# Kernel tuning notes

Measured on AMD Instinct MI355X. Metric: run time of the kernel, lower is better.

The kernel has to match this reference:

```python
import jax, jax.numpy as jnp
import numpy as np

M, N, H, K1, K2, C, B = 100000, 14000, 256, 16, 32, 7, 64
EPS = 1e-8


def setup_inputs() -> dict:
    key = jax.random.key(0)
    ks = jax.random.split(key, 8)
    embeds = jax.random.normal(ks[0], (M, H), dtype=jnp.float32)
    idx = jax.random.randint(ks[1], (N,), 0, M, dtype=jnp.int32)
    neighbors = jax.random.randint(ks[2], (N, K1), 0, M, dtype=jnp.int32)
    neighbors_2hop = jax.random.randint(ks[3], (N, K2), 0, M, dtype=jnp.int32)
    labels = (jnp.arange(N, dtype=jnp.int32) % C)  # perfectly balanced, as averageemb requires
    # prompt params (downstreamprompt weights, xavier-uniform [1,H])
    lim = float(np.sqrt(6.0 / (1 + H)))
    w_self = jax.random.uniform(ks[4], (1, H), jnp.float32, -lim, lim)
    w_n = jax.random.uniform(ks[5], (1, H), jnp.float32, -lim, lim)
    w_n2 = jax.random.uniform(ks[6], (1, H), jnp.float32, -lim, lim)
    # metanet (PromptVector): bottleneck adapter H -> B -> H
    k7, k8 = jax.random.split(ks[7])
    W1 = jax.random.normal(k7, (H, B), jnp.float32) * (1.0 / np.sqrt(H))
    b1 = jnp.zeros((B,), jnp.float32)
    W2 = jax.random.normal(k8, (B, H), jnp.float32) * (1.0 / np.sqrt(B))
    b2 = jnp.zeros((H,), jnp.float32)
    return {"embeds": embeds, "w_self": w_self, "w_n": w_n, "w_n2": w_n2,
            "W1": W1, "b1": b1, "W2": W2, "b2": b2,
            "idx": idx, "neighbors": neighbors, "neighbors_2hop": neighbors_2hop,
            "labels": labels}


def _cos(a, b):
    # torch.cosine_similarity with eps=1e-8 (clamped norms)
    num = jnp.sum(a * b, axis=-1)
    na = jnp.maximum(jnp.sqrt(jnp.sum(a * a, axis=-1)), EPS)
    nb = jnp.maximum(jnp.sqrt(jnp.sum(b * b, axis=-1)), EPS)
    return num / (na * nb)


def reference(embeds, w_self, w_n, w_n2, W1, b1, W2, b2,
              idx, neighbors, neighbors_2hop, labels):
    center = embeds[idx]                         # [N,H]
    ce = w_self * center                         # selfprompt: [N,H]
    nb = jnp.nan_to_num(w_n * embeds[neighbors])              # [N,K1,H]
    nb2 = jnp.nan_to_num(w_n2 * embeds[neighbors_2hop])       # [N,K2,H]
    nb_all = jnp.concatenate([nb, nb2], axis=1)  # [N,K1+K2,H]
    sim = _cos(ce[:, None, :], nb_all)           # [N,K]
    w = jax.nn.softmax(sim, axis=-1)
    weighted_neighbors = jnp.einsum('nk,nkh->nh', w, nb_all)
    inputs = weighted_neighbors + ce             # (dropout = identity at eval)
    prompts = jax.nn.elu(inputs @ W1 + b1) @ W2 + b2  # metanet adapter
    rawret = prompts + ce                        # [N,H]
    # averageemb: per-class mean (labels balanced, N/C per class)
    per_class = N // C
    ave = jax.ops.segment_sum(rawret, labels, num_segments=C) / per_class  # [C,H]
    ret = jax.nn.softmax(_cos(rawret[:, None, :], ave[None, :, :]), axis=1)  # [N,C]
    return ret
```

## Files before the change

### kernel.cpp

```cpp
#include <hip/hip_runtime.h>
#include <hip/hip_bf16.h>
#include <math.h>

#define H 256
#define NR 14000
#define MR 100000
#define K1C 16
#define K2C 32
#define KT 48
#define CC 7
#define EPSF 1e-8f
#define GC1 128
#define CHUNK ((NR + GC1 - 1) / GC1)

typedef __attribute__((ext_vector_type(8))) unsigned short ushort8_t;

__device__ __forceinline__ float rdlane(float v, int l) {
    return __int_as_float(__builtin_amdgcn_readlane(__float_as_int(v), l));
}

__device__ __forceinline__ float dot4(const float4 a, const float4 b) {
    return a.x * b.x + a.y * b.y + a.z * b.z + a.w * b.w;
}

__device__ __forceinline__ unsigned short f2bf(float x) {
    __hip_bfloat16 h = __float2bfloat16(x);
    return *(unsigned short*)&h;
}

__global__ __launch_bounds__(256) void kE(const float* __restrict__ src,
                                          unsigned short* __restrict__ dst) {
    const size_t base = ((size_t)blockIdx.x * 256 + threadIdx.x) * 8;
    const float4 a = *(const float4*)(src + base);
    const float4 b = *(const float4*)(src + base + 4);
    ushort8_t o;
    o[0] = f2bf(a.x); o[1] = f2bf(a.y); o[2] = f2bf(a.z); o[3] = f2bf(a.w);
    o[4] = f2bf(b.x); o[5] = f2bf(b.y); o[6] = f2bf(b.z); o[7] = f2bf(b.w);
    *(ushort8_t*)(dst + base) = o;
}

__global__ __launch_bounds__(256) void kA2(
    const float* __restrict__ embeds, const unsigned short* __restrict__ ebf,
    const float* __restrict__ w_self, const float* __restrict__ w_n,
    const float* __restrict__ w_n2, const int* __restrict__ idx,
    const int* __restrict__ nbr1, const int* __restrict__ nbr2,
    float* __restrict__ inbuf, float* __restrict__ cebuf)
{
    const int tid = threadIdx.x;
    const int wv = tid >> 6, lane = tid & 63;
    const int n = blockIdx.x * 4 + wv;
    const int g = lane >> 4, l = lane & 15;
    const int hb = l * 16;

    float ce[16], wn[16], wn2[16];
    float na2 = 0.f;
    const int cidx = idx[n];
    const float* crow = embeds + (size_t)cidx * H + hb;
#pragma unroll
    for (int j = 0; j < 4; ++j) {
        const float4 wsv  = *(const float4*)(w_self + hb + 4 * j);
        const float4 wnv  = *(const float4*)(w_n    + hb + 4 * j);
        const float4 wn2v = *(const float4*)(w_n2   + hb + 4 * j);
        const float4 cv   = *(const float4*)(crow + 4 * j);
        wn[4*j+0] = wnv.x;  wn[4*j+1] = wnv.y;  wn[4*j+2] = wnv.z;  wn[4*j+3] = wnv.w;
        wn2[4*j+0] = wn2v.x; wn2[4*j+1] = wn2v.y; wn2[4*j+2] = wn2v.z; wn2[4*j+3] = wn2v.w;
        ce[4*j+0] = wsv.x * cv.x; ce[4*j+1] = wsv.y * cv.y;
        ce[4*j+2] = wsv.z * cv.z; ce[4*j+3] = wsv.w * cv.w;
        na2 += ce[4*j+0]*ce[4*j+0] + ce[4*j+1]*ce[4*j+1]
             + ce[4*j+2]*ce[4*j+2] + ce[4*j+3]*ce[4*j+3];
    }
#pragma unroll
    for (int m = 1; m <= 8; m <<= 1) na2 += __shfl_xor(na2, m);
    const float na = fmaxf(sqrtf(na2), EPSF);

    int ridx = 0;
    if (lane < K1C) ridx = nbr1[n * K1C + lane];
    else if (lane < KT) ridx = nbr2[n * K2C + (lane - K1C)];

    float acc[16];
#pragma unroll
    for (int i = 0; i < 16; ++i) acc[i] = 0.f;
    float lsum = 0.f;

#pragma unroll
    for (int kk = 0; kk < 12; ++kk) {
        const int row = __shfl(ridx, kk * 4 + g);
        const unsigned short* rp = ebf + (size_t)row * H + hb;
        const ushort8_t e0 = *(const ushort8_t*)(rp);
        const ushort8_t e1 = *(const ushort8_t*)(rp + 8);
        float nb[16];
#pragma unroll
        for (int i = 0; i < 8; ++i) {
            nb[i]     = __uint_as_float((unsigned)e0[i] << 16);
            nb[8 + i] = __uint_as_float((unsigned)e1[i] << 16);
        }
        float num = 0.f, nn = 0.f;
#pragma unroll
        for (int i = 0; i < 16; ++i) {
            const float w = (kk < 4) ? wn[i] : wn2[i];
            nb[i] *= w;
            num += ce[i] * nb[i];
            nn  += nb[i] * nb[i];
        }
#pragma unroll
        for (int m = 1; m <= 8; m <<= 1) {
            num += __shfl_xor(num, m);
            nn  += __shfl_xor(nn, m);
        }
        const float nbn = fmaxf(sqrtf(nn), EPSF);
        const float e = __expf(num / (nbn * na) - 1.0f);
        lsum += e;
#pragma unroll
        for (int i = 0; i < 16; ++i) acc[i] += e * nb[i];
    }
#pragma unroll
    for (int m = 16; m <= 32; m <<= 1) {
        lsum += __shfl_xor(lsum, m);
#pragma unroll
        for (int i = 0; i < 16; ++i) acc[i] += __shfl_xor(acc[i], m);
    }
    const float rl = 1.0f / lsum;
    if (g == 0) {
        float* ip = inbuf + (size_t)n * H + hb;
        float* cp = cebuf + (size_t)n * H + hb;
#pragma unroll
        for (int i = 0; i < 16; ++i) {
            ip[i] = acc[i] * rl + ce[i];
            cp[i] = ce[i];
        }
    }
}

__global__ __launch_bounds__(256) void kA(
    const float* __restrict__ embeds, const float* __restrict__ w_self,
    const float* __restrict__ w_n, const float* __restrict__ w_n2,
    const int* __restrict__ idx, const int* __restrict__ nbr1,
    const int* __restrict__ nbr2, float* __restrict__ inbuf,
    float* __restrict__ cebuf)
{
    const int tid = threadIdx.x;
    const int wv = tid >> 6, lane = tid & 63;
    const int n = blockIdx.x * 4 + wv;
    const int g = lane >> 4, l = lane & 15;
    const int hb = l * 4;

    float4 wn4[4], wn24[4], ce4[4];
    float na2 = 0.f;
    const int cidx = idx[n];
    const float* crow = embeds + (size_t)cidx * H;
#pragma unroll
    for (int j = 0; j < 4; ++j) {
        const float4 wsv = *(const float4*)(w_self + hb + 64 * j);
        wn4[j]  = *(const float4*)(w_n  + hb + 64 * j);
        wn24[j] = *(const float4*)(w_n2 + hb + 64 * j);
        const float4 cv = *(const float4*)(crow + hb + 64 * j);
        float4 ce;
        ce.x = wsv.x * cv.x; ce.y = wsv.y * cv.y;
        ce.z = wsv.z * cv.z; ce.w = wsv.w * cv.w;
        ce4[j] = ce;
        na2 += dot4(ce, ce);
    }
#pragma unroll
    for (int m = 1; m <= 8; m <<= 1) na2 += __shfl_xor(na2, m);
    const float na = fmaxf(sqrtf(na2), EPSF);

    int ridx = 0;
    if (lane < K1C) ridx = nbr1[n * K1C + lane];
    else if (lane < KT) ridx = nbr2[n * K2C + (lane - K1C)];

    float4 acc[4];
#pragma unroll
    for (int j = 0; j < 4; ++j) acc[j] = make_float4(0.f, 0.f, 0.f, 0.f);
    float lsum = 0.f;

#pragma unroll
    for (int kk = 0; kk < 12; ++kk) {
        const int row = __shfl(ridx, kk * 4 + g);
        const float* rp = embeds + (size_t)row * H;
        float num = 0.f, nn = 0.f;
        float4 nb4[4];
#pragma unroll
        for (int j = 0; j < 4; ++j) {
            const float4 ev = *(const float4*)(rp + hb + 64 * j);
            const float4 wv4 = (kk < 4) ? wn4[j] : wn24[j];
            float4 nb;
            nb.x = wv4.x * ev.x; nb.y = wv4.y * ev.y;
            nb.z = wv4.z * ev.z; nb.w = wv4.w * ev.w;
            nb4[j] = nb;
            num += dot4(ce4[j], nb);
            nn  += dot4(nb, nb);
        }
#pragma unroll
        for (int m = 1; m <= 8; m <<= 1) {
            num += __shfl_xor(num, m);
            nn  += __shfl_xor(nn, m);
        }
        const float nbn = fmaxf(sqrtf(nn), EPSF);
        const float e = __expf(num / (nbn * na) - 1.0f);
        lsum += e;
#pragma unroll
        for (int j = 0; j < 4; ++j) {
            acc[j].x += e * nb4[j].x; acc[j].y += e * nb4[j].y;
            acc[j].z += e * nb4[j].z; acc[j].w += e * nb4[j].w;
        }
    }
#pragma unroll
    for (int m = 16; m <= 32; m <<= 1) {
        lsum += __shfl_xor(lsum, m);
#pragma unroll
        for (int j = 0; j < 4; ++j) {
            acc[j].x += __shfl_xor(acc[j].x, m);
            acc[j].y += __shfl_xor(acc[j].y, m);
            acc[j].z += __shfl_xor(acc[j].z, m);
            acc[j].w += __shfl_xor(acc[j].w, m);
        }
    }
    const float rl = 1.0f / lsum;
    if (g == 0) {
        float* ip = inbuf + (size_t)n * H;
        float* cp = cebuf + (size_t)n * H;
#pragma unroll
        for (int j = 0; j < 4; ++j) {
            float4 iv;
            iv.x = acc[j].x * rl + ce4[j].x;
            iv.y = acc[j].y * rl + ce4[j].y;
            iv.z = acc[j].z * rl + ce4[j].z;
            iv.w = acc[j].w * rl + ce4[j].w;
            *(float4*)(ip + hb + 64 * j) = iv;
            *(float4*)(cp + hb + 64 * j) = ce4[j];
        }
    }
}

__global__ __launch_bounds__(256) void kB2(
    float* __restrict__ io, const float* __restrict__ cebuf,
    const float* __restrict__ W1, const float* __restrict__ b1,
    const float* __restrict__ W2, const float* __restrict__ b2)
{
    const int tid = threadIdx.x;
    const int wv = tid >> 6, lane = tid & 63;
    const int r0 = __builtin_amdgcn_readfirstlane((blockIdx.x * 4 + wv) * 4);
    const float* inb = io + (size_t)r0 * H;

    float hid[4];
    const float bb = b1[lane];
#pragma unroll
    for (int r = 0; r < 4; ++r) hid[r] = bb;

#pragma unroll 8
    for (int h = 0; h < 256; ++h) {
        const float w1v = W1[h * 64 + lane];
        hid[0] += inb[h]           * w1v;
        hid[1] += inb[H + h]       * w1v;
        hid[2] += inb[2 * H + h]   * w1v;
        hid[3] += inb[3 * H + h]   * w1v;
    }
#pragma unroll
    for (int r = 0; r < 4; ++r)
        hid[r] = hid[r] > 0.f ? hid[r] : (__expf(hid[r]) - 1.0f);

    float4 p4[4];
    const float4 b2v = *(const float4*)(b2 + 4 * lane);
#pragma unroll
    for (int r = 0; r < 4; ++r) p4[r] = b2v;
#pragma unroll 4
    for (int b = 0; b < 64; ++b) {
        const float4 w2v = *(const float4*)(W2 + b * H + 4 * lane);
#pragma unroll
        for (int r = 0; r < 4; ++r) {
            const float hv = rdlane(hid[r], b);
            p4[r].x += hv * w2v.x; p4[r].y += hv * w2v.y;
            p4[r].z += hv * w2v.z; p4[r].w += hv * w2v.w;
        }
    }
#pragma unroll
    for (int r = 0; r < 4; ++r) {
        const float4 cev = *(const float4*)(cebuf + (size_t)(r0 + r) * H + 4 * lane);
        float4 ov;
        ov.x = p4[r].x + cev.x; ov.y = p4[r].y + cev.y;
        ov.z = p4[r].z + cev.z; ov.w = p4[r].w + cev.w;
        *(float4*)(io + (size_t)(r0 + r) * H + 4 * lane) = ov;
    }
}

__global__ __launch_bounds__(256) void kC1(
    const float* __restrict__ rawret, const int* __restrict__ labels,
    float* __restrict__ partial)
{
    const int t = threadIdx.x, j = blockIdx.x;
    const int nlo = j * CHUNK;
    const int nhi = min(nlo + CHUNK, NR);
    float acc[CC];
#pragma unroll
    for (int c = 0; c < CC; ++c) acc[c] = 0.f;
    for (int n = nlo; n < nhi; ++n) {
        const int lab = labels[n];
        const float v = rawret[(size_t)n * H + t];
#pragma unroll
        for (int c = 0; c < CC; ++c) acc[c] += (lab == c) ? v : 0.f;
    }
#pragma unroll
    for (int c = 0; c < CC; ++c) partial[(size_t)(j * CC + c) * H + t] = acc[c];
}

__global__ __launch_bounds__(256) void kC2(
    const float* __restrict__ partial, float* __restrict__ ave,
    float* __restrict__ anorm)
{
    const int c = blockIdx.x, t = threadIdx.x;
    float s = 0.f;
#pragma unroll 8
    for (int j = 0; j < GC1; ++j) s += partial[(size_t)(j * CC + c) * H + t];
    const float a = s * (1.0f / 2000.0f);
    ave[c * H + t] = a;
    __shared__ float red[256];
    red[t] = a * a;
    __syncthreads();
    for (int m = 128; m > 0; m >>= 1) {
        if (t < m) red[t] += red[t + m];
        __syncthreads();
    }
    if (t == 0) anorm[c] = fmaxf(sqrtf(red[0]), EPSF);
}

__global__ __launch_bounds__(256) void kD(
    const float* __restrict__ rawret, const float* __restrict__ ave,
    const float* __restrict__ anorm, float* __restrict__ out)
{
    const int tid = threadIdx.x;
    const int wv = tid >> 6, lane = tid & 63;
    const int n = blockIdx.x * 4 + wv;
    const float4 r4 = *(const float4*)(rawret + (size_t)n * H + 4 * lane);
    float nr2 = dot4(r4, r4);
#pragma unroll
    for (int m = 1; m <= 32; m <<= 1) nr2 += __shfl_xor(nr2, m);
    const float rn = fmaxf(sqrtf(nr2), EPSF);

    float e[CC];
    float s = 0.f;
#pragma unroll
    for (int c = 0; c < CC; ++c) {
        const float4 a4 = *(const float4*)(ave + c * H + 4 * lane);
        float d = dot4(r4, a4);
#pragma unroll
        for (int m = 1; m <= 32; m <<= 1) d += __shfl_xor(d, m);
        const float sim = d / (rn * anorm[c]);
        e[c] = __expf(sim - 1.0f);
        s += e[c];
    }
    const float rs = 1.0f / s;
    if (lane < CC) {
        float v = e[0];
#pragma unroll
        for (int c = 1; c < CC; ++c) v = (lane == c) ? e[c] : v;
        out[(size_t)n * CC + lane] = v * rs;
    }
}

extern "C" void kernel_launch(void* const* d_in, const int* in_sizes, int n_in,
                              void* d_out, int out_size, void* d_ws, size_t ws_size,
                              hipStream_t stream) {
    const float* embeds = (const float*)d_in[0];
    const float* w_self = (const float*)d_in[1];
    const float* w_n    = (const float*)d_in[2];
    const float* w_n2   = (const float*)d_in[3];
    const float* W1     = (const float*)d_in[4];
    const float* b1     = (const float*)d_in[5];
    const float* W2     = (const float*)d_in[6];
    const float* b2     = (const float*)d_in[7];
    const int* idx      = (const int*)d_in[8];
    const int* nbr1     = (const int*)d_in[9];
    const int* nbr2     = (const int*)d_in[10];
    const int* labels   = (const int*)d_in[11];
    float* out = (float*)d_out;

    float* buf0    = (float*)d_ws;
    float* buf1    = buf0 + (size_t)NR * H;
    float* partial = buf1 + (size_t)NR * H;
    float* ave     = partial + (size_t)GC1 * CC * H;
    float* anorm   = ave + (size_t)CC * H;
    unsigned short* ebf = (unsigned short*)(anorm + 8);

    const size_t need = ((char*)ebf - (char*)d_ws) + (size_t)MR * H * 2;

    if (ws_size >= need) {
        kE<<<(MR * H) / (256 * 8), 256, 0, stream>>>(embeds, ebf);
        kA2<<<NR / 4, 256, 0, stream>>>(embeds, ebf, w_self, w_n, w_n2,
                                        idx, nbr1, nbr2, buf0, buf1);
    } else {
        kA<<<NR / 4, 256, 0, stream>>>(embeds, w_self, w_n, w_n2,
                                       idx, nbr1, nbr2, buf0, buf1);
    }
    kB2<<<NR / 16, 256, 0, stream>>>(buf0, buf1, W1, b1, W2, b2);
    kC1<<<GC1, 256, 0, stream>>>(buf0, labels, partial);
    kC2<<<CC, 256, 0, stream>>>(partial, ave, anorm);
    kD<<<NR / 4, 256, 0, stream>>>(buf0, ave, anorm, out);
}
```

Baseline: 328.4 us.

## Fuse metanet adapter MLP into gather kernel and widen class-sum reduction grid

```diff
diff --git a/kernel.cpp b/kernel.cpp
--- a/kernel.cpp
+++ b/kernel.cpp
@@ -10,8 +10,8 @@
 #define KT 48
 #define CC 7
 #define EPSF 1e-8f
-#define GC1 128
-#define CHUNK ((NR + GC1 - 1) / GC1)
+#define GP 448
+#define CH2 32
 
 typedef __attribute__((ext_vector_type(8))) unsigned short ushort8_t;
 
@@ -39,12 +39,14 @@
     *(ushort8_t*)(dst + base) = o;
 }
 
-__global__ __launch_bounds__(256) void kA2(
+__global__ __launch_bounds__(256) void kA3(
     const float* __restrict__ embeds, const unsigned short* __restrict__ ebf,
     const float* __restrict__ w_self, const float* __restrict__ w_n,
     const float* __restrict__ w_n2, const int* __restrict__ idx,
     const int* __restrict__ nbr1, const int* __restrict__ nbr2,
-    float* __restrict__ inbuf, float* __restrict__ cebuf)
+    const float* __restrict__ W1, const float* __restrict__ b1,
+    const float* __restrict__ W2, const float* __restrict__ b2,
+    float* __restrict__ rawret)
 {
     const int tid = threadIdx.x;
     const int wv = tid >> 6, lane = tid & 63;
@@ -120,166 +122,57 @@
         for (int i = 0; i < 16; ++i) acc[i] += __shfl_xor(acc[i], m);
     }
     const float rl = 1.0f / lsum;
+    float inv[16];
+#pragma unroll
+    for (int i = 0; i < 16; ++i) inv[i] = acc[i] * rl + ce[i];
+
+    float hid = b1[lane];
+    const float* w1p = W1 + lane;
+#pragma unroll
+    for (int l2 = 0; l2 < 16; ++l2) {
+#pragma unroll
+        for (int i = 0; i < 16; ++i) {
+            const int h = 16 * l2 + i;
+            hid = fmaf(rdlane(inv[i], l2), w1p[h * 64], hid);
+        }
+    }
+    hid = hid > 0.f ? hid : (__expf(hid) - 1.0f);
+
+    float p[16];
+#pragma unroll
+    for (int i = 0; i < 16; ++i) p[i] = 0.f;
+    const int gb = lane & 48;
+#pragma unroll
+    for (int t = 0; t < 16; ++t) {
+        const float hv = __shfl(hid, gb + t);
+        const float* w2p = W2 + (size_t)(gb + t) * H + hb;
+#pragma unroll
+        for (int j = 0; j < 4; ++j) {
+            const float4 w2v = *(const float4*)(w2p + 4 * j);
+            p[4*j+0] = fmaf(hv, w2v.x, p[4*j+0]);
+            p[4*j+1] = fmaf(hv, w2v.y, p[4*j+1]);
+            p[4*j+2] = fmaf(hv, w2v.z, p[4*j+2]);
+            p[4*j+3] = fmaf(hv, w2v.w, p[4*j+3]);
+        }
+    }
+#pragma unroll
+    for (int m = 16; m <= 32; m <<= 1) {
+#pragma unroll
+        for (int i = 0; i < 16; ++i) p[i] += __shfl_xor(p[i], m);
+    }
+
     if (g == 0) {
-        float* ip = inbuf + (size_t)n * H + hb;
-        float* cp = cebuf + (size_t)n * H + hb;
-#pragma unroll
-        for (int i = 0; i < 16; ++i) {
-            ip[i] = acc[i] * rl + ce[i];
-            cp[i] = ce[i];
-        }
-    }
-}
-
-__global__ __launch_bounds__(256) void kA(
-    const float* __restrict__ embeds, const float* __restrict__ w_self,
-    const float* __restrict__ w_n, const float* __restrict__ w_n2,
-    const int* __restrict__ idx, const int* __restrict__ nbr1,
-    const int* __restrict__ nbr2, float* __restrict__ inbuf,
-    float* __restrict__ cebuf)
-{
-    const int tid = threadIdx.x;
-    const int wv = tid >> 6, lane = tid & 63;
-    const int n = blockIdx.x * 4 + wv;
-    const int g = lane >> 4, l = lane & 15;
-    const int hb = l * 4;
-
-    float4 wn4[4], wn24[4], ce4[4];
-    float na2 = 0.f;
-    const int cidx = idx[n];
-    const float* crow = embeds + (size_t)cidx * H;
-#pragma unroll
-    for (int j = 0; j < 4; ++j) {
-        const float4 wsv = *(const float4*)(w_self + hb + 64 * j);
-        wn4[j]  = *(const float4*)(w_n  + hb + 64 * j);
-        wn24[j] = *(const float4*)(w_n2 + hb + 64 * j);
-        const float4 cv = *(const float4*)(crow + hb + 64 * j);
-        float4 ce;
-        ce.x = wsv.x * cv.x; ce.y = wsv.y * cv.y;
-        ce.z = wsv.z * cv.z; ce.w = wsv.w * cv.w;
-        ce4[j] = ce;
-        na2 += dot4(ce, ce);
-    }
-#pragma unroll
-    for (int m = 1; m <= 8; m <<= 1) na2 += __shfl_xor(na2, m);
-    const float na = fmaxf(sqrtf(na2), EPSF);
-
-    int ridx = 0;
-    if (lane < K1C) ridx = nbr1[n * K1C + lane];
-    else if (lane < KT) ridx = nbr2[n * K2C + (lane - K1C)];
-
-    float4 acc[4];
-#pragma unroll
-    for (int j = 0; j < 4; ++j) acc[j] = make_float4(0.f, 0.f, 0.f, 0.f);
-    float lsum = 0.f;
-
-#pragma unroll
-    for (int kk = 0; kk < 12; ++kk) {
-        const int row = __shfl(ridx, kk * 4 + g);
-        const float* rp = embeds + (size_t)row * H;
-        float num = 0.f, nn = 0.f;
-        float4 nb4[4];
+        float* op = rawret + (size_t)n * H + hb;
 #pragma unroll
         for (int j = 0; j < 4; ++j) {
-            const float4 ev = *(const float4*)(rp + hb + 64 * j);
-            const float4 wv4 = (kk < 4) ? wn4[j] : wn24[j];
-            float4 nb;
-            nb.x = wv4.x * ev.x; nb.y = wv4.y * ev.y;
-            nb.z = wv4.z * ev.z; nb.w = wv4.w * ev.w;
-            nb4[j] = nb;
-            num += dot4(ce4[j], nb);
-            nn  += dot4(nb, nb);
-        }
-#pragma unroll
-        for (int m = 1; m <= 8; m <<= 1) {
-            num += __shfl_xor(num, m);
-            nn  += __shfl_xor(nn, m);
-        }
-        const float nbn = fmaxf(sqrtf(nn), EPSF);
-        const float e = __expf(num / (nbn * na) - 1.0f);
-        lsum += e;
-#pragma unroll
-        for (int j = 0; j < 4; ++j) {
-            acc[j].x += e * nb4[j].x; acc[j].y += e * nb4[j].y;
-            acc[j].z += e * nb4[j].z; acc[j].w += e * nb4[j].w;
-        }
-    }
-#pragma unroll
-    for (int m = 16; m <= 32; m <<= 1) {
-        lsum += __shfl_xor(lsum, m);
-#pragma unroll
-        for (int j = 0; j < 4; ++j) {
-            acc[j].x += __shfl_xor(acc[j].x, m);
-            acc[j].y += __shfl_xor(acc[j].y, m);
-            acc[j].z += __shfl_xor(acc[j].z, m);
-            acc[j].w += __shfl_xor(acc[j].w, m);
-        }
-    }
-    const float rl = 1.0f / lsum;
-    if (g == 0) {
-        float* ip = inbuf + (size_t)n * H;
-        float* cp = cebuf + (size_t)n * H;
-#pragma unroll
-        for (int j = 0; j < 4; ++j) {
-            float4 iv;
-            iv.x = acc[j].x * rl + ce4[j].x;
-            iv.y = acc[j].y * rl + ce4[j].y;
-            iv.z = acc[j].z * rl + ce4[j].z;
-            iv.w = acc[j].w * rl + ce4[j].w;
-            *(float4*)(ip + hb + 64 * j) = iv;
-            *(float4*)(cp + hb + 64 * j) = ce4[j];
-        }
-    }
-}
-
-__global__ __launch_bounds__(256) void kB2(
-    float* __restrict__ io, const float* __restrict__ cebuf,
-    const float* __restrict__ W1, const float* __restrict__ b1,
-    const float* __restrict__ W2, const float* __restrict__ b2)
-{
-    const int tid = threadIdx.x;
-    const int wv = tid >> 6, lane = tid & 63;
-    const int r0 = __builtin_amdgcn_readfirstlane((blockIdx.x * 4 + wv) * 4);
-    const float* inb = io + (size_t)r0 * H;
-
-    float hid[4];
-    const float bb = b1[lane];
-#pragma unroll
-    for (int r = 0; r < 4; ++r) hid[r] = bb;
-
-#pragma unroll 8
-    for (int h = 0; h < 256; ++h) {
-        const float w1v = W1[h * 64 + lane];
-        hid[0] += inb[h]           * w1v;
-        hid[1] += inb[H + h]       * w1v;
-        hid[2] += inb[2 * H + h]   * w1v;
-        hid[3] += inb[3 * H + h]   * w1v;
-    }
-#pragma unroll
-    for (int r = 0; r < 4; ++r)
-        hid[r] = hid[r] > 0.f ? hid[r] : (__expf(hid[r]) - 1.0f);
-
-    float4 p4[4];
-    const float4 b2v = *(const float4*)(b2 + 4 * lane);
-#pragma unroll
-    for (int r = 0; r < 4; ++r) p4[r] = b2v;
-#pragma unroll 4
-    for (int b = 0; b < 64; ++b) {
-        const float4 w2v = *(const float4*)(W2 + b * H + 4 * lane);
-#pragma unroll
-        for (int r = 0; r < 4; ++r) {
-            const float hv = rdlane(hid[r], b);
-            p4[r].x += hv * w2v.x; p4[r].y += hv * w2v.y;
-            p4[r].z += hv * w2v.z; p4[r].w += hv * w2v.w;
-        }
-    }
-#pragma unroll
-    for (int r = 0; r < 4; ++r) {
-        const float4 cev = *(const float4*)(cebuf + (size_t)(r0 + r) * H + 4 * lane);
-        float4 ov;
-        ov.x = p4[r].x + cev.x; ov.y = p4[r].y + cev.y;
-        ov.z = p4[r].z + cev.z; ov.w = p4[r].w + cev.w;
-        *(float4*)(io + (size_t)(r0 + r) * H + 4 * lane) = ov;
+            const float4 b2v = *(const float4*)(b2 + hb + 4 * j);
+            float4 ov;
+            ov.x = p[4*j+0] + b2v.x + ce[4*j+0];
+            ov.y = p[4*j+1] + b2v.y + ce[4*j+1];
+            ov.z = p[4*j+2] + b2v.z + ce[4*j+2];
+            ov.w = p[4*j+3] + b2v.w + ce[4*j+3];
+            *(float4*)(op + 4 * j) = ov;
+        }
     }
 }
 
@@ -288,16 +181,22 @@
     float* __restrict__ partial)
 {
     const int t = threadIdx.x, j = blockIdx.x;
-    const int nlo = j * CHUNK;
-    const int nhi = min(nlo + CHUNK, NR);
+    const int nlo = j * CH2;
+    const int nhi = min(nlo + CH2, NR);
     float acc[CC];
 #pragma unroll
     for (int c = 0; c < CC; ++c) acc[c] = 0.f;
-    for (int n = nlo; n < nhi; ++n) {
-        const int lab = labels[n];
-        const float v = rawret[(size_t)n * H + t];
-#pragma unroll
-        for (int c = 0; c < CC; ++c) acc[c] += (lab == c) ? v : 0.f;
+    for (int n = nlo; n < nhi; n += 4) {
+        int lab[4]; float v[4];
+#pragma unroll
+        for (int u = 0; u < 4; ++u) {
+            lab[u] = labels[n + u];
+            v[u] = rawret[(size_t)(n + u) * H + t];
+        }
+#pragma unroll
+        for (int u = 0; u < 4; ++u)
+#pragma unroll
+            for (int c = 0; c < CC; ++c) acc[c] += (lab[u] == c) ? v[u] : 0.f;
     }
 #pragma unroll
     for (int c = 0; c < CC; ++c) partial[(size_t)(j * CC + c) * H + t] = acc[c];
@@ -310,7 +209,7 @@
     const int c = blockIdx.x, t = threadIdx.x;
     float s = 0.f;
 #pragma unroll 8
-    for (int j = 0; j < GC1; ++j) s += partial[(size_t)(j * CC + c) * H + t];
+    for (int j = 0; j < GP; ++j) s += partial[(size_t)(j * CC + c) * H + t];
     const float a = s * (1.0f / 2000.0f);
     ave[c * H + t] = a;
     __shared__ float red[256];
@@ -374,25 +273,16 @@
     const int* labels   = (const int*)d_in[11];
     float* out = (float*)d_out;
 
-    float* buf0    = (float*)d_ws;
-    float* buf1    = buf0 + (size_t)NR * H;
-    float* partial = buf1 + (size_t)NR * H;
-    float* ave     = partial + (size_t)GC1 * CC * H;
+    float* rawret  = (float*)d_ws;
+    float* partial = rawret + (size_t)NR * H;
+    float* ave     = partial + (size_t)GP * CC * H;
     float* anorm   = ave + (size_t)CC * H;
     unsigned short* ebf = (unsigned short*)(anorm + 8);
 
-    const size_t need = ((char*)ebf - (char*)d_ws) + (size_t)MR * H * 2;
-
-    if (ws_size >= need) {
-        kE<<<(MR * H) / (256 * 8), 256, 0, stream>>>(embeds, ebf);
-        kA2<<<NR / 4, 256, 0, stream>>>(embeds, ebf, w_self, w_n, w_n2,
-                                        idx, nbr1, nbr2, buf0, buf1);
-    } else {
-        kA<<<NR / 4, 256, 0, stream>>>(embeds, w_self, w_n, w_n2,
-                                       idx, nbr1, nbr2, buf0, buf1);
-    }
-    kB2<<<NR / 16, 256, 0, stream>>>(buf0, buf1, W1, b1, W2, b2);
-    kC1<<<GC1, 256, 0, stream>>>(buf0, labels, partial);
+    kE<<<(MR * H) / (256 * 8), 256, 0, stream>>>(embeds, ebf);
+    kA3<<<NR / 4, 256, 0, stream>>>(embeds, ebf, w_self, w_n, w_n2,
+                                    idx, nbr1, nbr2, W1, b1, W2, b2, rawret);
+    kC1<<<GP, 256, 0, stream>>>(rawret, labels, partial);
     kC2<<<CC, 256, 0, stream>>>(partial, ave, anorm);
-    kD<<<NR / 4, 256, 0, stream>>>(buf0, ave, anorm, out);
-}
+    kD<<<NR / 4, 256, 0, stream>>>(rawret, ave, anorm, out);
+}
```

New measurement: 358.6 us. +9.2%, slower.
